# Performance work log

Hardware: AMD Instinct MI355X
Metric: run time of the kernel (lower is better)

The kernel has to match this reference:

```python
import jax, jax.numpy as jnp
import numpy as np

COST_LABELS = 2.0
COST_BBOX = 5.0
COST_GIOU = 2.0
NUM_HEADS = 7
NUM_CLASSES = 16


def setup_inputs() -> dict:
    key = jax.random.key(0)
    k0, k1, k2, k3 = jax.random.split(key, 4)
    bs, nq, nt = 16, 900, 100
    return {
        "pred_logits": jax.random.normal(k0, (NUM_HEADS, bs, nq, NUM_CLASSES), jnp.float32),
        "pred_boxes": jax.random.uniform(k1, (bs, nq, 4), jnp.float32),
        "tgt_boxes": jax.random.uniform(k2, (bs, nt, 4), jnp.float32),
        "tgt_labels": jax.random.randint(k3, (NUM_HEADS, bs, nt), 0, NUM_CLASSES),
    }


def box_cxcywh_to_xyxy(b):
    cx, cy, w, h = jnp.split(b, 4, axis=-1)
    return jnp.concatenate([cx - 0.5 * w, cy - 0.5 * h, cx + 0.5 * w, cy + 0.5 * h], axis=-1)


def generalized_box_iou(a, b):
    # a: [N,4] xyxy, b: [M,4] xyxy -> [N,M]
    area_a = (a[:, 2] - a[:, 0]) * (a[:, 3] - a[:, 1])
    area_b = (b[:, 2] - b[:, 0]) * (b[:, 3] - b[:, 1])
    lt = jnp.maximum(a[:, None, :2], b[None, :, :2])
    rb = jnp.minimum(a[:, None, 2:], b[None, :, 2:])
    wh = jnp.clip(rb - lt, 0.0)
    inter = wh[..., 0] * wh[..., 1]
    union = area_a[:, None] + area_b[None, :] - inter
    iou = inter / union
    lt_e = jnp.minimum(a[:, None, :2], b[None, :, :2])
    rb_e = jnp.maximum(a[:, None, 2:], b[None, :, 2:])
    wh_e = jnp.clip(rb_e - lt_e, 0.0)
    area = wh_e[..., 0] * wh_e[..., 1]
    return iou - (area - union) / area


@jax.jit
def compute_cost(pred_logits, pred_boxes, tgt_boxes, tgt_labels):
    bs, nq, _ = pred_boxes.shape
    out_bbox = pred_boxes.reshape(-1, 4)   # [N,4] cxcywh
    tgt_bbox = tgt_boxes.reshape(-1, 4)    # [M,4] cxcywh
    # L1 cdist
    cost_bbox = jnp.sum(jnp.abs(out_bbox[:, None, :] - tgt_bbox[None, :, :]), axis=-1)
    cost_giou = -generalized_box_iou(box_cxcywh_to_xyxy(out_bbox), box_cxcywh_to_xyxy(tgt_bbox))
    # label cost: sum over the 7 heads of -sigmoid(logits)[:, tgt_ids]
    probs = jax.nn.sigmoid(pred_logits.reshape(NUM_HEADS, -1, NUM_CLASSES))  # [7,N,C]
    ids = tgt_labels.reshape(NUM_HEADS, -1)                                   # [7,M]
    cost_labels = jnp.zeros_like(cost_bbox)
    for h in range(NUM_HEADS):  # small fixed loop, avoids a [7,N,M] intermediate
        cost_labels = cost_labels - probs[h][:, ids[h]]
    C = COST_BBOX * cost_bbox + COST_LABELS * cost_labels + COST_GIOU * cost_giou
    return C.reshape(bs, nq, -1)  # [bs, nq, bs*nt]


def _lsa(cost):
    """Jonker-Volgenant shortest augmenting path. cost: [r,c] with r<=c.
    Returns row2col: optimal column for each row (minimizes total cost)."""
    cost = np.asarray(cost, dtype=np.float64)
    r, c = cost.shape
    u = np.zeros(r + 1)
    v = np.zeros(c + 1)
    p = np.zeros(c + 1, np.int64)    # p[j] = row matched to column j (1-indexed)
    way = np.zeros(c + 1, np.int64)
    for i in range(1, r + 1):
        p[0] = i
        j0 = 0
        minv = np.full(c + 1, np.inf)
        used = np.zeros(c + 1, bool)
        while True:
            used[j0] = True
            i0 = p[j0]
            free = np.nonzero(~used)[0]  # unused columns (1..c)
            cur = cost[i0 - 1, free - 1] - u[i0] - v[free]
            better = cur < minv[free]
            minv[free] = np.where(better, cur, minv[free])
            way[free[better]] = j0
            k = np.argmin(minv[free])
            j1 = free[k]
            delta = minv[free][k]
            u[p[used]] += delta
            v[used] -= delta
            minv[free] -= delta
            j0 = j1
            if p[j0] == 0:
                break
        while j0:
            j1 = way[j0]
            p[j0] = p[j1]
            j0 = j1
    row2col = np.full(r, -1, np.int64)
    for j in range(1, c + 1):
        if p[j] > 0:
            row2col[p[j] - 1] = j - 1
    return row2col


def reference(pred_logits, pred_boxes, tgt_boxes, tgt_labels):
    C = compute_cost(pred_logits, pred_boxes, tgt_boxes, tgt_labels)  # [bs, nq, bs*nt]
    bs, nq, M = C.shape
    nt = M // bs
    Cn = np.asarray(C)
    out = np.zeros((bs, 2, nt), np.int64)
    for b in range(bs):
        sub = Cn[b, :, b * nt:(b + 1) * nt]  # [nq, nt] per-image block (mimics C.split(sizes))
        t2p = _lsa(sub.T)                    # for each target, its matched prediction
        order = np.argsort(t2p, kind="stable")  # scipy returns row indices sorted
        out[b, 0] = t2p[order]  # index_i: selected predictions (sorted)
        out[b, 1] = order       # index_j: corresponding targets
    return jnp.asarray(out)
```

## Files before the change

### kernel.cpp

```cpp
#include <hip/hip_runtime.h>
#include <hip/hip_bf16.h>
#include <math.h>

#define NQ 900
#define NT 100
#define BS 16
#define NH 7
#define NC 16
#define SLOTS 15

__global__ __launch_bounds__(256) void sig_transpose_kernel(const float* __restrict__ logits,
                                                            float* __restrict__ probsT) {
    const int hb = blockIdx.x;
    const float* src = logits + (size_t)hb * NQ * NC;
    float* dst = probsT + (size_t)hb * NC * NQ;
    __shared__ float tile[NC][NQ + 1];
    for (int e = threadIdx.x; e < NQ * NC; e += 256) {
        int q = e >> 4, c = e & 15;
        float x = src[e];
        tile[c][q] = 1.0f / (1.0f + expf(-x));
    }
    __syncthreads();
    for (int c = 0; c < NC; ++c)
        for (int q = threadIdx.x; q < NQ; q += 256)
            dst[c * NQ + q] = tile[c][q];
}

__global__ __launch_bounds__(256) void cost_kernel2(const float4* __restrict__ pboxes4,
                                                    const float4* __restrict__ tboxes4,
                                                    const int*    __restrict__ tlabels,
                                                    const float*  __restrict__ probsT,
                                                    float* __restrict__ costT) {
    int id = blockIdx.x * 256 + threadIdx.x;
    if (id >= BS * NT * NQ) return;
    int q = id % NQ;
    int t = (id / NQ) % NT;
    int b = id / (NQ * NT);

    float4 pb = pboxes4[b * NQ + q];
    float4 tb = tboxes4[b * NT + t];
    float px = pb.x, py = pb.y, pw = pb.z, ph = pb.w;
    float tx = tb.x, ty = tb.y, tw = tb.z, th = tb.w;

    float cost_bbox = fabsf(px - tx) + fabsf(py - ty) + fabsf(pw - tw) + fabsf(ph - th);

    float ax0 = px - 0.5f * pw, ay0 = py - 0.5f * ph;
    float ax1 = px + 0.5f * pw, ay1 = py + 0.5f * ph;
    float bx0 = tx - 0.5f * tw, by0 = ty - 0.5f * th;
    float bx1 = tx + 0.5f * tw, by1 = ty + 0.5f * th;
    float areaA = (ax1 - ax0) * (ay1 - ay0);
    float areaB = (bx1 - bx0) * (by1 - by0);
    float ltx = fmaxf(ax0, bx0), lty = fmaxf(ay0, by0);
    float rbx = fminf(ax1, bx1), rby = fminf(ay1, by1);
    float iw = fmaxf(rbx - ltx, 0.f), ih = fmaxf(rby - lty, 0.f);
    float inter = iw * ih;
    float uni = areaA + areaB - inter;
    float iou = inter / uni;
    float ex0 = fminf(ax0, bx0), ey0 = fminf(ay0, by0);
    float ex1 = fmaxf(ax1, bx1), ey1 = fmaxf(ay1, by1);
    float ew = fmaxf(ex1 - ex0, 0.f), eh = fmaxf(ey1 - ey0, 0.f);
    float earea = ew * eh;
    float giou = iou - (earea - uni) / earea;

    float ssum = 0.f;
    #pragma unroll
    for (int h = 0; h < NH; ++h) {
        int lab = tlabels[(h * BS + b) * NT + t];
        ssum += probsT[(size_t)((h * BS + b) * NC + lab) * NQ + q];
    }

    costT[(b * NT + t) * NQ + q] = 5.0f * cost_bbox - 2.0f * ssum - 2.0f * giou;
}

__global__ void cost_kernel_fb(const float* __restrict__ logits,
                               const float* __restrict__ pboxes,
                               const float* __restrict__ tboxes,
                               const int*   __restrict__ tlabels,
                               float* __restrict__ costT) {
    int id = blockIdx.x * blockDim.x + threadIdx.x;
    if (id >= BS * NT * NQ) return;
    int q = id % NQ;
    int t = (id / NQ) % NT;
    int b = id / (NQ * NT);

    const float* pb = pboxes + (b * NQ + q) * 4;
    const float* tb = tboxes + (b * NT + t) * 4;
    float px = pb[0], py = pb[1], pw = pb[2], ph = pb[3];
    float tx = tb[0], ty = tb[1], tw = tb[2], th = tb[3];

    float cost_bbox = fabsf(px - tx) + fabsf(py - ty) + fabsf(pw - tw) + fabsf(ph - th);

    float ax0 = px - 0.5f * pw, ay0 = py - 0.5f * ph;
    float ax1 = px + 0.5f * pw, ay1 = py + 0.5f * ph;
    float bx0 = tx - 0.5f * tw, by0 = ty - 0.5f * th;
    float bx1 = tx + 0.5f * tw, by1 = ty + 0.5f * th;
    float areaA = (ax1 - ax0) * (ay1 - ay0);
    float areaB = (bx1 - bx0) * (by1 - by0);
    float ltx = fmaxf(ax0, bx0), lty = fmaxf(ay0, by0);
    float rbx = fminf(ax1, bx1), rby = fminf(ay1, by1);
    float iw = fmaxf(rbx - ltx, 0.f), ih = fmaxf(rby - lty, 0.f);
    float inter = iw * ih;
    float uni = areaA + areaB - inter;
    float iou = inter / uni;
    float ex0 = fminf(ax0, bx0), ey0 = fminf(ay0, by0);
    float ex1 = fmaxf(ax1, bx1), ey1 = fmaxf(ay1, by1);
    float ew = fmaxf(ex1 - ex0, 0.f), eh = fmaxf(ey1 - ey0, 0.f);
    float earea = ew * eh;
    float giou = iou - (earea - uni) / earea;

    float ssum = 0.f;
    #pragma unroll
    for (int h = 0; h < NH; ++h) {
        int lab = tlabels[(h * BS + b) * NT + t];
        float x = logits[((h * BS + b) * NQ + q) * NC + lab];
        ssum += 1.0f / (1.0f + expf(-x));
    }

    costT[(b * NT + t) * NQ + q] = 5.0f * cost_bbox - 2.0f * ssum - 2.0f * giou;
}

__global__ __launch_bounds__(64) void lsa_kernel(const float* __restrict__ costT,
                                                 int* __restrict__ out) {
    const int b = blockIdx.x;
    const int lane = threadIdx.x;
    const float* cost = costT + b * NT * NQ;

    __shared__ double u_s[NT + 1];
    __shared__ int p_s[NQ + 1];
    __shared__ int way_s[NQ + 1];
    __shared__ int r2c[NT];
    __shared__ int jmin_s[NT];
    __shared__ int unass[NT];
    __shared__ int nun_s;

    for (int j = lane; j <= NQ; j += 64) p_s[j] = 0;
    __syncthreads();

    for (int base = 0; base < NT; base += 64) {
        int r = base + lane;
        if (r < NT) {
            const float4* row4 = (const float4*)(cost + (size_t)r * NQ);
            float m0 = INFINITY, m1 = INFINITY, m2 = INFINITY, m3 = INFINITY;
            int i0 = 0, i1 = 0, i2 = 0, i3 = 0;
            #pragma unroll 5
            for (int q4 = 0; q4 < NQ / 4; ++q4) {
                float4 cv = row4[q4];
                if (cv.x < m0) { m0 = cv.x; i0 = 4 * q4; }
                if (cv.y < m1) { m1 = cv.y; i1 = 4 * q4 + 1; }
                if (cv.z < m2) { m2 = cv.z; i2 = 4 * q4 + 2; }
                if (cv.w < m3) { m3 = cv.w; i3 = 4 * q4 + 3; }
            }
            float mv = m0; int mj = i0;
            if (m1 < mv || (m1 == mv && i1 < mj)) { mv = m1; mj = i1; }
            if (m2 < mv || (m2 == mv && i2 < mj)) { mv = m2; mj = i2; }
            if (m3 < mv || (m3 == mv && i3 < mj)) { mv = m3; mj = i3; }
            u_s[r + 1] = (double)mv;
            jmin_s[r] = mj;
        }
    }
    __syncthreads();

    if (lane == 0) {
        int nun = 0;
        for (int i = 1; i <= NT; ++i) {
            int j = jmin_s[i - 1] + 1;
            if (p_s[j] == 0) p_s[j] = i;
            else unass[nun++] = i;
        }
        nun_s = nun;
    }
    __syncthreads();
    const int nun = nun_s;

    double v[SLOTS], minv[SLOTS], ureg[SLOTS];
    int pof[SLOTS];
    #pragma unroll
    for (int k = 0; k < SLOTS; ++k) { v[k] = 0.0; ureg[k] = 0.0; pof[k] = 0; }
    const unsigned invalid = (lane < 4) ? 0u : (1u << 14);
    double u_c0 = 0.0;

    for (int ii = 0; ii < nun; ++ii) {
        const int i = unass[ii];
        #pragma unroll
        for (int k = 0; k < SLOTS; ++k) minv[k] = INFINITY;
        unsigned used = invalid;
        int j0 = 0;
        int i0 = i;

        while (true) {
            double u_i0 = u_s[i0];
            if (j0 != 0) {
                if (lane == ((j0 - 1) & 63)) {
                    int slot = (j0 - 1) >> 6;
                    used |= (1u << slot);
                    #pragma unroll
                    for (int k = 0; k < SLOTS; ++k)
                        if (slot == k) { pof[k] = i0; ureg[k] = u_i0; }
                }
            } else {
                if (lane == 0) u_c0 = u_i0;
            }

            const float* crow = cost + (size_t)(i0 - 1) * NQ;
            float c[SLOTS];
            #pragma unroll
            for (int k = 0; k < SLOTS - 1; ++k) c[k] = crow[lane + 64 * k];
            c[SLOTS - 1] = (lane < 4) ? crow[lane + 64 * (SLOTS - 1)] : 0.0f;

            double bv = INFINITY;
            int bj = 2048;
            #pragma unroll
            for (int k = 0; k < SLOTS; ++k) {
                if (!((used >> k) & 1u)) {
                    int j = 1 + lane + 64 * k;
                    double cur = ((double)c[k] - u_i0) - v[k];
                    if (cur < minv[k]) { minv[k] = cur; way_s[j] = j0; }
                    if (minv[k] < bv) { bv = minv[k]; bj = j; }
                }
            }
            #pragma unroll
            for (int off = 1; off < 64; off <<= 1) {
                double ov = __shfl_xor(bv, off);
                int oj = __shfl_xor(bj, off);
                if (ov < bv || (ov == bv && oj < bj)) { bv = ov; bj = oj; }
            }
            const double delta = bv;

            #pragma unroll
            for (int k = 0; k < SLOTS; ++k) {
                if ((used >> k) & 1u) { ureg[k] += delta; v[k] -= delta; }
                else                  { minv[k] -= delta; }
            }
            if (lane == 0) u_c0 += delta;

            j0 = bj;
            int pj = p_s[j0];
            if (pj == 0) break;
            i0 = pj;
        }

        __syncthreads();
        if (lane == 0) {
            int j = j0;
            while (j) {
                int jw = way_s[j];
                p_s[j] = (jw == 0) ? i : p_s[jw];
                j = jw;
            }
            u_s[i] = u_c0;
        }
        #pragma unroll
        for (int k = 0; k < SLOTS; ++k) {
            if (((used >> k) & 1u) && !((invalid >> k) & 1u)) u_s[pof[k]] = ureg[k];
        }
        __syncthreads();
    }

    for (int j = 1 + lane; j <= NQ; j += 64) {
        int pi = p_s[j];
        if (pi > 0) r2c[pi - 1] = j - 1;
    }
    __syncthreads();
    for (int t = lane; t < NT; t += 64) {
        int ccol = r2c[t];
        int rank = 0;
        for (int tt = 0; tt < NT; ++tt) rank += (r2c[tt] < ccol) ? 1 : 0;
        out[b * 2 * NT + rank] = ccol;
        out[b * 2 * NT + NT + rank] = t;
    }
}

extern "C" void kernel_launch(void* const* d_in, const int* in_sizes, int n_in,
                              void* d_out, int out_size, void* d_ws, size_t ws_size,
                              hipStream_t stream) {
    const float* logits  = (const float*)d_in[0];
    const float* pboxes  = (const float*)d_in[1];
    const float* tboxes  = (const float*)d_in[2];
    const int*   tlabels = (const int*)d_in[3];
    int* out = (int*)d_out;
    float* costT = (float*)d_ws;

    const size_t costT_elems  = (size_t)BS * NT * NQ;
    const size_t probsT_elems = (size_t)NH * BS * NC * NQ;
    const size_t need = (costT_elems + probsT_elems) * sizeof(float);

    const int total = BS * NT * NQ;
    if (ws_size >= need) {
        float* probsT = costT + costT_elems;
        sig_transpose_kernel<<<NH * BS, 256, 0, stream>>>(logits, probsT);
        cost_kernel2<<<(total + 255) / 256, 256, 0, stream>>>(
            (const float4*)pboxes, (const float4*)tboxes, tlabels, probsT, costT);
    } else {
        cost_kernel_fb<<<(total + 255) / 256, 256, 0, stream>>>(logits, pboxes, tboxes, tlabels, costT);
    }
    lsa_kernel<<<BS, 64, 0, stream>>>(costT, out);
}
```

Baseline: 128.5 us.

## Add auction-style augmenting row reduction before shortest-path LSA and fuse cost kernels

```diff
diff --git a/kernel.cpp b/kernel.cpp
--- a/kernel.cpp
+++ b/kernel.cpp
@@ -8,115 +8,57 @@
 #define NH 7
 #define NC 16
 #define SLOTS 15
-
-__global__ __launch_bounds__(256) void sig_transpose_kernel(const float* __restrict__ logits,
-                                                            float* __restrict__ probsT) {
-    const int hb = blockIdx.x;
-    const float* src = logits + (size_t)hb * NQ * NC;
-    float* dst = probsT + (size_t)hb * NC * NQ;
-    __shared__ float tile[NC][NQ + 1];
-    for (int e = threadIdx.x; e < NQ * NC; e += 256) {
-        int q = e >> 4, c = e & 15;
-        float x = src[e];
-        tile[c][q] = 1.0f / (1.0f + expf(-x));
-    }
-    __syncthreads();
-    for (int c = 0; c < NC; ++c)
-        for (int q = threadIdx.x; q < NQ; q += 256)
-            dst[c * NQ + q] = tile[c][q];
-}
-
-__global__ __launch_bounds__(256) void cost_kernel2(const float4* __restrict__ pboxes4,
-                                                    const float4* __restrict__ tboxes4,
-                                                    const int*    __restrict__ tlabels,
-                                                    const float*  __restrict__ probsT,
-                                                    float* __restrict__ costT) {
-    int id = blockIdx.x * 256 + threadIdx.x;
-    if (id >= BS * NT * NQ) return;
-    int q = id % NQ;
-    int t = (id / NQ) % NT;
-    int b = id / (NQ * NT);
-
-    float4 pb = pboxes4[b * NQ + q];
+#define MAXARR 512
+#define MAXTREE 8192
+
+__global__ __launch_bounds__(256) void cost_kernel(const float*  __restrict__ logits,
+                                                   const float4* __restrict__ pboxes4,
+                                                   const float4* __restrict__ tboxes4,
+                                                   const int*    __restrict__ tlabels,
+                                                   float* __restrict__ costT) {
+    const int bt = blockIdx.x;
+    const int b = bt / NT, t = bt % NT;
+
+    int lab[NH];
+    #pragma unroll
+    for (int h = 0; h < NH; ++h) lab[h] = tlabels[(h * BS + b) * NT + t];
+
     float4 tb = tboxes4[b * NT + t];
-    float px = pb.x, py = pb.y, pw = pb.z, ph = pb.w;
     float tx = tb.x, ty = tb.y, tw = tb.z, th = tb.w;
-
-    float cost_bbox = fabsf(px - tx) + fabsf(py - ty) + fabsf(pw - tw) + fabsf(ph - th);
-
-    float ax0 = px - 0.5f * pw, ay0 = py - 0.5f * ph;
-    float ax1 = px + 0.5f * pw, ay1 = py + 0.5f * ph;
     float bx0 = tx - 0.5f * tw, by0 = ty - 0.5f * th;
     float bx1 = tx + 0.5f * tw, by1 = ty + 0.5f * th;
-    float areaA = (ax1 - ax0) * (ay1 - ay0);
     float areaB = (bx1 - bx0) * (by1 - by0);
-    float ltx = fmaxf(ax0, bx0), lty = fmaxf(ay0, by0);
-    float rbx = fminf(ax1, bx1), rby = fminf(ay1, by1);
-    float iw = fmaxf(rbx - ltx, 0.f), ih = fmaxf(rby - lty, 0.f);
-    float inter = iw * ih;
-    float uni = areaA + areaB - inter;
-    float iou = inter / uni;
-    float ex0 = fminf(ax0, bx0), ey0 = fminf(ay0, by0);
-    float ex1 = fmaxf(ax1, bx1), ey1 = fmaxf(ay1, by1);
-    float ew = fmaxf(ex1 - ex0, 0.f), eh = fmaxf(ey1 - ey0, 0.f);
-    float earea = ew * eh;
-    float giou = iou - (earea - uni) / earea;
-
-    float ssum = 0.f;
-    #pragma unroll
-    for (int h = 0; h < NH; ++h) {
-        int lab = tlabels[(h * BS + b) * NT + t];
-        ssum += probsT[(size_t)((h * BS + b) * NC + lab) * NQ + q];
-    }
-
-    costT[(b * NT + t) * NQ + q] = 5.0f * cost_bbox - 2.0f * ssum - 2.0f * giou;
-}
-
-__global__ void cost_kernel_fb(const float* __restrict__ logits,
-                               const float* __restrict__ pboxes,
-                               const float* __restrict__ tboxes,
-                               const int*   __restrict__ tlabels,
-                               float* __restrict__ costT) {
-    int id = blockIdx.x * blockDim.x + threadIdx.x;
-    if (id >= BS * NT * NQ) return;
-    int q = id % NQ;
-    int t = (id / NQ) % NT;
-    int b = id / (NQ * NT);
-
-    const float* pb = pboxes + (b * NQ + q) * 4;
-    const float* tb = tboxes + (b * NT + t) * 4;
-    float px = pb[0], py = pb[1], pw = pb[2], ph = pb[3];
-    float tx = tb[0], ty = tb[1], tw = tb[2], th = tb[3];
-
-    float cost_bbox = fabsf(px - tx) + fabsf(py - ty) + fabsf(pw - tw) + fabsf(ph - th);
-
-    float ax0 = px - 0.5f * pw, ay0 = py - 0.5f * ph;
-    float ax1 = px + 0.5f * pw, ay1 = py + 0.5f * ph;
-    float bx0 = tx - 0.5f * tw, by0 = ty - 0.5f * th;
-    float bx1 = tx + 0.5f * tw, by1 = ty + 0.5f * th;
-    float areaA = (ax1 - ax0) * (ay1 - ay0);
-    float areaB = (bx1 - bx0) * (by1 - by0);
-    float ltx = fmaxf(ax0, bx0), lty = fmaxf(ay0, by0);
-    float rbx = fminf(ax1, bx1), rby = fminf(ay1, by1);
-    float iw = fmaxf(rbx - ltx, 0.f), ih = fmaxf(rby - lty, 0.f);
-    float inter = iw * ih;
-    float uni = areaA + areaB - inter;
-    float iou = inter / uni;
-    float ex0 = fminf(ax0, bx0), ey0 = fminf(ay0, by0);
-    float ex1 = fmaxf(ax1, bx1), ey1 = fmaxf(ay1, by1);
-    float ew = fmaxf(ex1 - ex0, 0.f), eh = fmaxf(ey1 - ey0, 0.f);
-    float earea = ew * eh;
-    float giou = iou - (earea - uni) / earea;
-
-    float ssum = 0.f;
-    #pragma unroll
-    for (int h = 0; h < NH; ++h) {
-        int lab = tlabels[(h * BS + b) * NT + t];
-        float x = logits[((h * BS + b) * NQ + q) * NC + lab];
-        ssum += 1.0f / (1.0f + expf(-x));
-    }
-
-    costT[(b * NT + t) * NQ + q] = 5.0f * cost_bbox - 2.0f * ssum - 2.0f * giou;
+
+    for (int q = threadIdx.x; q < NQ; q += 256) {
+        float4 pb = pboxes4[b * NQ + q];
+        float px = pb.x, py = pb.y, pw = pb.z, ph = pb.w;
+
+        float cost_bbox = fabsf(px - tx) + fabsf(py - ty) + fabsf(pw - tw) + fabsf(ph - th);
+
+        float ax0 = px - 0.5f * pw, ay0 = py - 0.5f * ph;
+        float ax1 = px + 0.5f * pw, ay1 = py + 0.5f * ph;
+        float areaA = (ax1 - ax0) * (ay1 - ay0);
+        float ltx = fmaxf(ax0, bx0), lty = fmaxf(ay0, by0);
+        float rbx = fminf(ax1, bx1), rby = fminf(ay1, by1);
+        float iw = fmaxf(rbx - ltx, 0.f), ih = fmaxf(rby - lty, 0.f);
+        float inter = iw * ih;
+        float uni = areaA + areaB - inter;
+        float iou = inter / uni;
+        float ex0 = fminf(ax0, bx0), ey0 = fminf(ay0, by0);
+        float ex1 = fmaxf(ax1, bx1), ey1 = fmaxf(ay1, by1);
+        float ew = fmaxf(ex1 - ex0, 0.f), eh = fmaxf(ey1 - ey0, 0.f);
+        float earea = ew * eh;
+        float giou = iou - (earea - uni) / earea;
+
+        float ssum = 0.f;
+        #pragma unroll
+        for (int h = 0; h < NH; ++h) {
+            float x = logits[(size_t)((h * BS + b) * NQ + q) * NC + lab[h]];
+            ssum += 1.0f / (1.0f + expf(-x));
+        }
+
+        costT[(b * NT + t) * NQ + q] = 5.0f * cost_bbox - 2.0f * ssum - 2.0f * giou;
+    }
 }
 
 __global__ __launch_bounds__(64) void lsa_kernel(const float* __restrict__ costT,
@@ -125,35 +67,36 @@
     const int lane = threadIdx.x;
     const float* cost = costT + b * NT * NQ;
 
+    __shared__ double2 pu[NQ + 1];
     __shared__ double u_s[NT + 1];
-    __shared__ int p_s[NQ + 1];
     __shared__ int way_s[NQ + 1];
-    __shared__ int r2c[NT];
+    __shared__ int x_s[NT + 1];
     __shared__ int jmin_s[NT];
     __shared__ int unass[NT];
+    __shared__ int r2c[NT];
     __shared__ int nun_s;
 
-    for (int j = lane; j <= NQ; j += 64) p_s[j] = 0;
+    for (int j = lane; j <= NQ; j += 64) pu[j] = make_double2(0.0, 0.0);
     __syncthreads();
 
     for (int base = 0; base < NT; base += 64) {
         int r = base + lane;
         if (r < NT) {
             const float4* row4 = (const float4*)(cost + (size_t)r * NQ);
-            float m0 = INFINITY, m1 = INFINITY, m2 = INFINITY, m3 = INFINITY;
+            float m0 = INFINITY, m1f = INFINITY, m2f = INFINITY, m3f = INFINITY;
             int i0 = 0, i1 = 0, i2 = 0, i3 = 0;
             #pragma unroll 5
             for (int q4 = 0; q4 < NQ / 4; ++q4) {
                 float4 cv = row4[q4];
-                if (cv.x < m0) { m0 = cv.x; i0 = 4 * q4; }
-                if (cv.y < m1) { m1 = cv.y; i1 = 4 * q4 + 1; }
-                if (cv.z < m2) { m2 = cv.z; i2 = 4 * q4 + 2; }
-                if (cv.w < m3) { m3 = cv.w; i3 = 4 * q4 + 3; }
+                if (cv.x < m0)  { m0 = cv.x;  i0 = 4 * q4; }
+                if (cv.y < m1f) { m1f = cv.y; i1 = 4 * q4 + 1; }
+                if (cv.z < m2f) { m2f = cv.z; i2 = 4 * q4 + 2; }
+                if (cv.w < m3f) { m3f = cv.w; i3 = 4 * q4 + 3; }
             }
             float mv = m0; int mj = i0;
-            if (m1 < mv || (m1 == mv && i1 < mj)) { mv = m1; mj = i1; }
-            if (m2 < mv || (m2 == mv && i2 < mj)) { mv = m2; mj = i2; }
-            if (m3 < mv || (m3 == mv && i3 < mj)) { mv = m3; mj = i3; }
+            if (m1f < mv || (m1f == mv && i1 < mj)) { mv = m1f; mj = i1; }
+            if (m2f < mv || (m2f == mv && i2 < mj)) { mv = m2f; mj = i2; }
+            if (m3f < mv || (m3f == mv && i3 < mj)) { mv = m3f; mj = i3; }
             u_s[r + 1] = (double)mv;
             jmin_s[r] = mj;
         }
@@ -164,8 +107,8 @@
         int nun = 0;
         for (int i = 1; i <= NT; ++i) {
             int j = jmin_s[i - 1] + 1;
-            if (p_s[j] == 0) p_s[j] = i;
-            else unass[nun++] = i;
+            if ((int)pu[j].y == 0) { pu[j] = make_double2(u_s[i], (double)i); x_s[i] = j; }
+            else                   { x_s[i] = 0; unass[nun++] = i; }
         }
         nun_s = nun;
     }
@@ -179,16 +122,80 @@
     const unsigned invalid = (lane < 4) ? 0u : (1u << 14);
     double u_c0 = 0.0;
 
-    for (int ii = 0; ii < nun; ++ii) {
+    {
+        int steps = 0;
+        for (int idx = 0; idx < nun; ++idx) {
+            int i = unass[idx];
+            while (i != 0 && steps < MAXARR) {
+                ++steps;
+                const float* crow = cost + (size_t)(i - 1) * NQ;
+                float c[SLOTS];
+                #pragma unroll
+                for (int k = 0; k < SLOTS - 1; ++k) c[k] = crow[lane + 64 * k];
+                c[SLOTS - 1] = (lane < 4) ? crow[lane + 64 * (SLOTS - 1)] : 0.0f;
+
+                double m1 = INFINITY, m2 = INFINITY;
+                int j1 = 2048;
+                #pragma unroll
+                for (int k = 0; k < SLOTS; ++k) {
+                    if (!((invalid >> k) & 1u)) {
+                        int j = 1 + lane + 64 * k;
+                        double d = (double)c[k] - v[k];
+                        if (d < m1 || (d == m1 && j < j1)) { m2 = m1; m1 = d; j1 = j; }
+                        else if (d < m2) m2 = d;
+                    }
+                }
+                #pragma unroll
+                for (int off = 1; off < 64; off <<= 1) {
+                    double om1 = __shfl_xor(m1, off);
+                    double om2 = __shfl_xor(m2, off);
+                    int oj1 = __shfl_xor(j1, off);
+                    if (om1 < m1 || (om1 == m1 && oj1 < j1)) { m2 = fmin(m1, om2); m1 = om1; j1 = oj1; }
+                    else { m2 = fmin(m2, om1); }
+                }
+
+                double2 t = pu[j1];
+                int k1 = (int)t.y;
+                if (m1 == m2 && k1 != 0) break;
+
+                if (m1 < m2) {
+                    if (lane == ((j1 - 1) & 63)) {
+                        int slot = (j1 - 1) >> 6;
+                        #pragma unroll
+                        for (int k = 0; k < SLOTS; ++k) if (k == slot) v[k] -= (m2 - m1);
+                    }
+                }
+                if (lane == 0) {
+                    u_s[i] = m2;
+                    pu[j1] = make_double2(m2, (double)i);
+                    x_s[i] = j1;
+                    if (k1) x_s[k1] = 0;
+                }
+                i = k1;
+            }
+        }
+    }
+    __syncthreads();
+
+    if (lane == 0) {
+        int n2 = 0;
+        for (int i = 1; i <= NT; ++i) if (x_s[i] == 0) unass[n2++] = i;
+        nun_s = n2;
+    }
+    __syncthreads();
+    const int nun2 = nun_s;
+
+    for (int ii = 0; ii < nun2; ++ii) {
         const int i = unass[ii];
         #pragma unroll
         for (int k = 0; k < SLOTS; ++k) minv[k] = INFINITY;
         unsigned used = invalid;
         int j0 = 0;
         int i0 = i;
-
-        while (true) {
-            double u_i0 = u_s[i0];
+        double u_i0 = u_s[i];
+        int guard = 0;
+
+        while (guard++ < MAXTREE) {
             if (j0 != 0) {
                 if (lane == ((j0 - 1) & 63)) {
                     int slot = (j0 - 1) >> 6;
@@ -233,31 +240,38 @@
             }
             if (lane == 0) u_c0 += delta;
 
+            double2 t = pu[bj];
             j0 = bj;
-            int pj = p_s[j0];
-            if (pj == 0) break;
-            i0 = pj;
-        }
-
+            i0 = (int)t.y;
+            u_i0 = t.x;
+            if (i0 == 0) break;
+        }
+
+        __syncthreads();
+        #pragma unroll
+        for (int k = 0; k < SLOTS; ++k) {
+            if (((used >> k) & 1u) && !((invalid >> k) & 1u)) {
+                int j = 1 + lane + 64 * k;
+                u_s[pof[k]] = ureg[k];
+                pu[j] = make_double2(ureg[k], (double)pof[k]);
+            }
+        }
         __syncthreads();
         if (lane == 0) {
+            u_s[i] = u_c0;
             int j = j0;
             while (j) {
                 int jw = way_s[j];
-                p_s[j] = (jw == 0) ? i : p_s[jw];
+                double2 t2 = (jw == 0) ? make_double2(u_c0, (double)i) : pu[jw];
+                pu[j] = t2;
                 j = jw;
             }
-            u_s[i] = u_c0;
-        }
-        #pragma unroll
-        for (int k = 0; k < SLOTS; ++k) {
-            if (((used >> k) & 1u) && !((invalid >> k) & 1u)) u_s[pof[k]] = ureg[k];
         }
         __syncthreads();
     }
 
     for (int j = 1 + lane; j <= NQ; j += 64) {
-        int pi = p_s[j];
+        int pi = (int)pu[j].y;
         if (pi > 0) r2c[pi - 1] = j - 1;
     }
     __syncthreads();
@@ -280,18 +294,7 @@
     int* out = (int*)d_out;
     float* costT = (float*)d_ws;
 
-    const size_t costT_elems  = (size_t)BS * NT * NQ;
-    const size_t probsT_elems = (size_t)NH * BS * NC * NQ;
-    const size_t need = (costT_elems + probsT_elems) * sizeof(float);
-
-    const int total = BS * NT * NQ;
-    if (ws_size >= need) {
-        float* probsT = costT + costT_elems;
-        sig_transpose_kernel<<<NH * BS, 256, 0, stream>>>(logits, probsT);
-        cost_kernel2<<<(total + 255) / 256, 256, 0, stream>>>(
-            (const float4*)pboxes, (const float4*)tboxes, tlabels, probsT, costT);
-    } else {
-        cost_kernel_fb<<<(total + 255) / 256, 256, 0, stream>>>(logits, pboxes, tboxes, tlabels, costT);
-    }
+    cost_kernel<<<BS * NT, 256, 0, stream>>>(logits, (const float4*)pboxes,
+                                             (const float4*)tboxes, tlabels, costT);
     lsa_kernel<<<BS, 64, 0, stream>>>(costT, out);
 }
```

After: 147.3 us. +14.6%, slower.

## Add auction-style reduction-transfer pre-pass and per-target cost kernel blocks

Applied to the files above, without the earlier changes.

```diff
diff --git a/kernel.cpp b/kernel.cpp
--- a/kernel.cpp
+++ b/kernel.cpp
@@ -8,6 +8,8 @@
 #define NH 7
 #define NC 16
 #define SLOTS 15
+#define MAXROUNDS 32
+#define MAXTREE 8192
 
 __global__ __launch_bounds__(256) void sig_transpose_kernel(const float* __restrict__ logits,
                                                             float* __restrict__ probsT) {
@@ -26,21 +28,71 @@
             dst[c * NQ + q] = tile[c][q];
 }
 
-__global__ __launch_bounds__(256) void cost_kernel2(const float4* __restrict__ pboxes4,
-                                                    const float4* __restrict__ tboxes4,
-                                                    const int*    __restrict__ tlabels,
-                                                    const float*  __restrict__ probsT,
-                                                    float* __restrict__ costT) {
-    int id = blockIdx.x * 256 + threadIdx.x;
+__global__ __launch_bounds__(256) void cost_kernel_bt(const float4* __restrict__ pboxes4,
+                                                      const float4* __restrict__ tboxes4,
+                                                      const int*    __restrict__ tlabels,
+                                                      const float*  __restrict__ probsT,
+                                                      float* __restrict__ costT) {
+    const int bt = blockIdx.x;
+    const int b = bt / NT, t = bt % NT;
+
+    const float* prow[NH];
+    #pragma unroll
+    for (int h = 0; h < NH; ++h) {
+        int lab = tlabels[(h * BS + b) * NT + t];
+        prow[h] = probsT + (size_t)((h * BS + b) * NC + lab) * NQ;
+    }
+
+    float4 tb = tboxes4[b * NT + t];
+    float tx = tb.x, ty = tb.y, tw = tb.z, th = tb.w;
+    float bx0 = tx - 0.5f * tw, by0 = ty - 0.5f * th;
+    float bx1 = tx + 0.5f * tw, by1 = ty + 0.5f * th;
+    float areaB = (bx1 - bx0) * (by1 - by0);
+
+    for (int q = threadIdx.x; q < NQ; q += 256) {
+        float4 pb = pboxes4[b * NQ + q];
+        float px = pb.x, py = pb.y, pw = pb.z, ph = pb.w;
+
+        float cost_bbox = fabsf(px - tx) + fabsf(py - ty) + fabsf(pw - tw) + fabsf(ph - th);
+
+        float ax0 = px - 0.5f * pw, ay0 = py - 0.5f * ph;
+        float ax1 = px + 0.5f * pw, ay1 = py + 0.5f * ph;
+        float areaA = (ax1 - ax0) * (ay1 - ay0);
+        float ltx = fmaxf(ax0, bx0), lty = fmaxf(ay0, by0);
+        float rbx = fminf(ax1, bx1), rby = fminf(ay1, by1);
+        float iw = fmaxf(rbx - ltx, 0.f), ih = fmaxf(rby - lty, 0.f);
+        float inter = iw * ih;
+        float uni = areaA + areaB - inter;
+        float iou = inter / uni;
+        float ex0 = fminf(ax0, bx0), ey0 = fminf(ay0, by0);
+        float ex1 = fmaxf(ax1, bx1), ey1 = fmaxf(ay1, by1);
+        float ew = fmaxf(ex1 - ex0, 0.f), eh = fmaxf(ey1 - ey0, 0.f);
+        float earea = ew * eh;
+        float giou = iou - (earea - uni) / earea;
+
+        float ssum = 0.f;
+        #pragma unroll
+        for (int h = 0; h < NH; ++h) ssum += prow[h][q];
+
+        costT[(b * NT + t) * NQ + q] = 5.0f * cost_bbox - 2.0f * ssum - 2.0f * giou;
+    }
+}
+
+__global__ void cost_kernel_fb(const float* __restrict__ logits,
+                               const float* __restrict__ pboxes,
+                               const float* __restrict__ tboxes,
+                               const int*   __restrict__ tlabels,
+                               float* __restrict__ costT) {
+    int id = blockIdx.x * blockDim.x + threadIdx.x;
     if (id >= BS * NT * NQ) return;
     int q = id % NQ;
     int t = (id / NQ) % NT;
     int b = id / (NQ * NT);
 
-    float4 pb = pboxes4[b * NQ + q];
-    float4 tb = tboxes4[b * NT + t];
-    float px = pb.x, py = pb.y, pw = pb.z, ph = pb.w;
-    float tx = tb.x, ty = tb.y, tw = tb.z, th = tb.w;
+    const float* pb = pboxes + (b * NQ + q) * 4;
+    const float* tb = tboxes + (b * NT + t) * 4;
+    float px = pb[0], py = pb[1], pw = pb[2], ph = pb[3];
+    float tx = tb[0], ty = tb[1], tw = tb[2], th = tb[3];
 
     float cost_bbox = fabsf(px - tx) + fabsf(py - ty) + fabsf(pw - tw) + fabsf(ph - th);
 
@@ -66,52 +118,6 @@
     #pragma unroll
     for (int h = 0; h < NH; ++h) {
         int lab = tlabels[(h * BS + b) * NT + t];
-        ssum += probsT[(size_t)((h * BS + b) * NC + lab) * NQ + q];
-    }
-
-    costT[(b * NT + t) * NQ + q] = 5.0f * cost_bbox - 2.0f * ssum - 2.0f * giou;
-}
-
-__global__ void cost_kernel_fb(const float* __restrict__ logits,
-                               const float* __restrict__ pboxes,
-                               const float* __restrict__ tboxes,
-                               const int*   __restrict__ tlabels,
-                               float* __restrict__ costT) {
-    int id = blockIdx.x * blockDim.x + threadIdx.x;
-    if (id >= BS * NT * NQ) return;
-    int q = id % NQ;
-    int t = (id / NQ) % NT;
-    int b = id / (NQ * NT);
-
-    const float* pb = pboxes + (b * NQ + q) * 4;
-    const float* tb = tboxes + (b * NT + t) * 4;
-    float px = pb[0], py = pb[1], pw = pb[2], ph = pb[3];
-    float tx = tb[0], ty = tb[1], tw = tb[2], th = tb[3];
-
-    float cost_bbox = fabsf(px - tx) + fabsf(py - ty) + fabsf(pw - tw) + fabsf(ph - th);
-
-    float ax0 = px - 0.5f * pw, ay0 = py - 0.5f * ph;
-    float ax1 = px + 0.5f * pw, ay1 = py + 0.5f * ph;
-    float bx0 = tx - 0.5f * tw, by0 = ty - 0.5f * th;
-    float bx1 = tx + 0.5f * tw, by1 = ty + 0.5f * th;
-    float areaA = (ax1 - ax0) * (ay1 - ay0);
-    float areaB = (bx1 - bx0) * (by1 - by0);
-    float ltx = fmaxf(ax0, bx0), lty = fmaxf(ay0, by0);
-    float rbx = fminf(ax1, bx1), rby = fminf(ay1, by1);
-    float iw = fmaxf(rbx - ltx, 0.f), ih = fmaxf(rby - lty, 0.f);
-    float inter = iw * ih;
-    float uni = areaA + areaB - inter;
-    float iou = inter / uni;
-    float ex0 = fminf(ax0, bx0), ey0 = fminf(ay0, by0);
-    float ex1 = fmaxf(ax1, bx1), ey1 = fmaxf(ay1, by1);
-    float ew = fmaxf(ex1 - ex0, 0.f), eh = fmaxf(ey1 - ey0, 0.f);
-    float earea = ew * eh;
-    float giou = iou - (earea - uni) / earea;
-
-    float ssum = 0.f;
-    #pragma unroll
-    for (int h = 0; h < NH; ++h) {
-        int lab = tlabels[(h * BS + b) * NT + t];
         float x = logits[((h * BS + b) * NQ + q) * NC + lab];
         ssum += 1.0f / (1.0f + expf(-x));
     }
@@ -125,52 +131,68 @@
     const int lane = threadIdx.x;
     const float* cost = costT + b * NT * NQ;
 
+    __shared__ double2 pu[NQ + 1];
     __shared__ double u_s[NT + 1];
-    __shared__ int p_s[NQ + 1];
     __shared__ int way_s[NQ + 1];
+    __shared__ int x_s[NT + 1];
+    __shared__ int p_w[NQ + 1];
+    __shared__ int touched[NQ + 1];
+    __shared__ int jmin_s[NT];
+    __shared__ int listA[NT], listB[NT];
+    __shared__ double2 scan_mm[NT];
+    __shared__ int scan_j1[NT];
     __shared__ int r2c[NT];
-    __shared__ int jmin_s[NT];
-    __shared__ int unass[NT];
-    __shared__ int nun_s;
-
-    for (int j = lane; j <= NQ; j += 64) p_s[j] = 0;
+    __shared__ int cnt_s;
+
+    for (int j = lane; j <= NQ; j += 64) {
+        pu[j] = make_double2(0.0, 0.0);
+        p_w[j] = 0x7fffffff;
+        touched[j] = -1;
+    }
+    if (lane == 0) cnt_s = 0;
     __syncthreads();
 
     for (int base = 0; base < NT; base += 64) {
         int r = base + lane;
         if (r < NT) {
             const float4* row4 = (const float4*)(cost + (size_t)r * NQ);
-            float m0 = INFINITY, m1 = INFINITY, m2 = INFINITY, m3 = INFINITY;
+            float m0 = INFINITY, m1f = INFINITY, m2f = INFINITY, m3f = INFINITY;
             int i0 = 0, i1 = 0, i2 = 0, i3 = 0;
             #pragma unroll 5
             for (int q4 = 0; q4 < NQ / 4; ++q4) {
                 float4 cv = row4[q4];
-                if (cv.x < m0) { m0 = cv.x; i0 = 4 * q4; }
-                if (cv.y < m1) { m1 = cv.y; i1 = 4 * q4 + 1; }
-                if (cv.z < m2) { m2 = cv.z; i2 = 4 * q4 + 2; }
-                if (cv.w < m3) { m3 = cv.w; i3 = 4 * q4 + 3; }
+                if (cv.x < m0)  { m0 = cv.x;  i0 = 4 * q4; }
+                if (cv.y < m1f) { m1f = cv.y; i1 = 4 * q4 + 1; }
+                if (cv.z < m2f) { m2f = cv.z; i2 = 4 * q4 + 2; }
+                if (cv.w < m3f) { m3f = cv.w; i3 = 4 * q4 + 3; }
             }
             float mv = m0; int mj = i0;
-            if (m1 < mv || (m1 == mv && i1 < mj)) { mv = m1; mj = i1; }
-            if (m2 < mv || (m2 == mv && i2 < mj)) { mv = m2; mj = i2; }
-            if (m3 < mv || (m3 == mv && i3 < mj)) { mv = m3; mj = i3; }
+            if (m1f < mv || (m1f == mv && i1 < mj)) { mv = m1f; mj = i1; }
+            if (m2f < mv || (m2f == mv && i2 < mj)) { mv = m2f; mj = i2; }
+            if (m3f < mv || (m3f == mv && i3 < mj)) { mv = m3f; mj = i3; }
             u_s[r + 1] = (double)mv;
             jmin_s[r] = mj;
-        }
-    }
-    __syncthreads();
-
-    if (lane == 0) {
-        int nun = 0;
-        for (int i = 1; i <= NT; ++i) {
-            int j = jmin_s[i - 1] + 1;
-            if (p_s[j] == 0) p_s[j] = i;
-            else unass[nun++] = i;
-        }
-        nun_s = nun;
-    }
-    __syncthreads();
-    const int nun = nun_s;
+            atomicMin(&p_w[mj + 1], r + 1);
+        }
+    }
+    __syncthreads();
+
+    for (int base = 0; base < NT; base += 64) {
+        int r = base + lane;
+        if (r < NT) {
+            int j = jmin_s[r] + 1;
+            if (p_w[j] == r + 1) {
+                x_s[r + 1] = j;
+                pu[j] = make_double2(u_s[r + 1], (double)(r + 1));
+            } else {
+                x_s[r + 1] = 0;
+                int pos = atomicAdd(&cnt_s, 1);
+                listA[pos] = r + 1;
+            }
+        }
+    }
+    __syncthreads();
+    int nfree = cnt_s;
 
     double v[SLOTS], minv[SLOTS], ureg[SLOTS];
     int pof[SLOTS];
@@ -179,16 +201,112 @@
     const unsigned invalid = (lane < 4) ? 0u : (1u << 14);
     double u_c0 = 0.0;
 
-    for (int ii = 0; ii < nun; ++ii) {
-        const int i = unass[ii];
+    int* curL = listA;
+    int* nxtL = listB;
+    for (int round = 0; round < MAXROUNDS && nfree > 0; ++round) {
+        for (int idx = 0; idx < nfree; idx += 2) {
+            const int iA = curL[idx];
+            const bool hasB = (idx + 1) < nfree;
+            const int iB = hasB ? curL[idx + 1] : iA;
+            const float* rowA = cost + (size_t)(iA - 1) * NQ;
+            const float* rowB = cost + (size_t)(iB - 1) * NQ;
+            float cA[SLOTS], cB[SLOTS];
+            #pragma unroll
+            for (int k = 0; k < SLOTS - 1; ++k) cA[k] = rowA[lane + 64 * k];
+            cA[SLOTS - 1] = (lane < 4) ? rowA[lane + 64 * (SLOTS - 1)] : 0.0f;
+            #pragma unroll
+            for (int k = 0; k < SLOTS - 1; ++k) cB[k] = rowB[lane + 64 * k];
+            cB[SLOTS - 1] = (lane < 4) ? rowB[lane + 64 * (SLOTS - 1)] : 0.0f;
+
+            {
+                double m1 = INFINITY, m2 = INFINITY; int j1 = 2048;
+                #pragma unroll
+                for (int k = 0; k < SLOTS; ++k) {
+                    if (!((invalid >> k) & 1u)) {
+                        int j = 1 + lane + 64 * k;
+                        double d = (double)cA[k] - v[k];
+                        if (d < m1 || (d == m1 && j < j1)) { m2 = m1; m1 = d; j1 = j; }
+                        else if (d < m2) m2 = d;
+                    }
+                }
+                #pragma unroll
+                for (int off = 1; off < 64; off <<= 1) {
+                    double om1 = __shfl_xor(m1, off);
+                    double om2 = __shfl_xor(m2, off);
+                    int oj1 = __shfl_xor(j1, off);
+                    if (om1 < m1 || (om1 == m1 && oj1 < j1)) { m2 = fmin(m1, om2); m1 = om1; j1 = oj1; }
+                    else m2 = fmin(m2, om1);
+                }
+                if (lane == 0) { scan_mm[idx] = make_double2(m1, m2); scan_j1[idx] = j1; }
+            }
+            if (hasB) {
+                double m1 = INFINITY, m2 = INFINITY; int j1 = 2048;
+                #pragma unroll
+                for (int k = 0; k < SLOTS; ++k) {
+                    if (!((invalid >> k) & 1u)) {
+                        int j = 1 + lane + 64 * k;
+                        double d = (double)cB[k] - v[k];
+                        if (d < m1 || (d == m1 && j < j1)) { m2 = m1; m1 = d; j1 = j; }
+                        else if (d < m2) m2 = d;
+                    }
+                }
+                #pragma unroll
+                for (int off = 1; off < 64; off <<= 1) {
+                    double om1 = __shfl_xor(m1, off);
+                    double om2 = __shfl_xor(m2, off);
+                    int oj1 = __shfl_xor(j1, off);
+                    if (om1 < m1 || (om1 == m1 && oj1 < j1)) { m2 = fmin(m1, om2); m1 = om1; j1 = oj1; }
+                    else m2 = fmin(m2, om1);
+                }
+                if (lane == 0) { scan_mm[idx + 1] = make_double2(m1, m2); scan_j1[idx + 1] = j1; }
+            }
+        }
+
+        int nfree2 = 0;
+        for (int idx = 0; idx < nfree; ++idx) {
+            int i = curL[idx];
+            double2 mm = scan_mm[idx];
+            int j1 = scan_j1[idx];
+            if (touched[j1] == round) {
+                if (lane == 0) nxtL[nfree2] = i;
+                ++nfree2;
+                continue;
+            }
+            int k1 = (int)pu[j1].y;
+            if (lane == 0) touched[j1] = round;
+            int sl = (j1 - 1) >> 6;
+            if (lane == ((j1 - 1) & 63)) {
+                double dv = mm.y - mm.x;
+                #pragma unroll
+                for (int k = 0; k < SLOTS; ++k) if (k == sl) v[k] -= dv;
+            }
+            if (lane == 0) {
+                u_s[i] = mm.y;
+                pu[j1] = make_double2(mm.y, (double)i);
+                x_s[i] = j1;
+                if (k1) x_s[k1] = 0;
+            }
+            if (k1) {
+                if (lane == 0) nxtL[nfree2] = k1;
+                ++nfree2;
+            }
+        }
+        int* tmp = curL; curL = nxtL; nxtL = tmp;
+        nfree = nfree2;
+    }
+    __syncthreads();
+
+    for (int ii = 0; ii < nfree; ++ii) {
+        const int i = curL[ii];
         #pragma unroll
         for (int k = 0; k < SLOTS; ++k) minv[k] = INFINITY;
         unsigned used = invalid;
         int j0 = 0;
         int i0 = i;
-
-        while (true) {
-            double u_i0 = u_s[i0];
+        double u_i0 = u_s[i];
+        int guard = 0;
+
+        while (guard++ < MAXTREE) {
             if (j0 != 0) {
                 if (lane == ((j0 - 1) & 63)) {
                     int slot = (j0 - 1) >> 6;
@@ -233,31 +351,38 @@
             }
             if (lane == 0) u_c0 += delta;
 
+            double2 t = pu[bj];
             j0 = bj;
-            int pj = p_s[j0];
-            if (pj == 0) break;
-            i0 = pj;
-        }
-
+            i0 = (int)t.y;
+            u_i0 = t.x;
+            if (i0 == 0) break;
+        }
+
+        __syncthreads();
+        #pragma unroll
+        for (int k = 0; k < SLOTS; ++k) {
+            if (((used >> k) & 1u) && !((invalid >> k) & 1u)) {
+                int j = 1 + lane + 64 * k;
+                u_s[pof[k]] = ureg[k];
+                pu[j] = make_double2(ureg[k], (double)pof[k]);
+            }
+        }
         __syncthreads();
         if (lane == 0) {
+            u_s[i] = u_c0;
             int j = j0;
             while (j) {
                 int jw = way_s[j];
-                p_s[j] = (jw == 0) ? i : p_s[jw];
+                double2 t2 = (jw == 0) ? make_double2(u_c0, (double)i) : pu[jw];
+                pu[j] = t2;
                 j = jw;
             }
-            u_s[i] = u_c0;
-        }
-        #pragma unroll
-        for (int k = 0; k < SLOTS; ++k) {
-            if (((used >> k) & 1u) && !((invalid >> k) & 1u)) u_s[pof[k]] = ureg[k];
         }
         __syncthreads();
     }
 
     for (int j = 1 + lane; j <= NQ; j += 64) {
-        int pi = p_s[j];
+        int pi = (int)pu[j].y;
         if (pi > 0) r2c[pi - 1] = j - 1;
     }
     __syncthreads();
@@ -284,13 +409,13 @@
     const size_t probsT_elems = (size_t)NH * BS * NC * NQ;
     const size_t need = (costT_elems + probsT_elems) * sizeof(float);
 
-    const int total = BS * NT * NQ;
     if (ws_size >= need) {
         float* probsT = costT + costT_elems;
         sig_transpose_kernel<<<NH * BS, 256, 0, stream>>>(logits, probsT);
-        cost_kernel2<<<(total + 255) / 256, 256, 0, stream>>>(
-            (const float4*)pboxes, (const float4*)tboxes, tlabels, probsT, costT);
+        cost_kernel_bt<<<BS * NT, 256, 0, stream>>>((const float4*)pboxes,
+                                                    (const float4*)tboxes, tlabels, probsT, costT);
     } else {
+        const int total = BS * NT * NQ;
         cost_kernel_fb<<<(total + 255) / 256, 256, 0, stream>>>(logits, pboxes, tboxes, tlabels, costT);
     }
     lsa_kernel<<<BS, 64, 0, stream>>>(costT, out);
```

New measurement: 133.8 us. 1.04x slower.

## Pack assignment and dual into shared double2; parallelize greedy init; per-target cost blocks

Applied to the files above, without the earlier changes.

```diff
diff --git a/kernel.cpp b/kernel.cpp
--- a/kernel.cpp
+++ b/kernel.cpp
@@ -8,6 +8,7 @@
 #define NH 7
 #define NC 16
 #define SLOTS 15
+#define MAXTREE 8192
 
 __global__ __launch_bounds__(256) void sig_transpose_kernel(const float* __restrict__ logits,
                                                             float* __restrict__ probsT) {
@@ -26,21 +27,71 @@
             dst[c * NQ + q] = tile[c][q];
 }
 
-__global__ __launch_bounds__(256) void cost_kernel2(const float4* __restrict__ pboxes4,
-                                                    const float4* __restrict__ tboxes4,
-                                                    const int*    __restrict__ tlabels,
-                                                    const float*  __restrict__ probsT,
-                                                    float* __restrict__ costT) {
-    int id = blockIdx.x * 256 + threadIdx.x;
+__global__ __launch_bounds__(256) void cost_kernel_bt(const float4* __restrict__ pboxes4,
+                                                      const float4* __restrict__ tboxes4,
+                                                      const int*    __restrict__ tlabels,
+                                                      const float*  __restrict__ probsT,
+                                                      float* __restrict__ costT) {
+    const int bt = blockIdx.x;
+    const int b = bt / NT, t = bt % NT;
+
+    const float* prow[NH];
+    #pragma unroll
+    for (int h = 0; h < NH; ++h) {
+        int lab = tlabels[(h * BS + b) * NT + t];
+        prow[h] = probsT + (size_t)((h * BS + b) * NC + lab) * NQ;
+    }
+
+    float4 tb = tboxes4[b * NT + t];
+    float tx = tb.x, ty = tb.y, tw = tb.z, th = tb.w;
+    float bx0 = tx - 0.5f * tw, by0 = ty - 0.5f * th;
+    float bx1 = tx + 0.5f * tw, by1 = ty + 0.5f * th;
+    float areaB = (bx1 - bx0) * (by1 - by0);
+
+    for (int q = threadIdx.x; q < NQ; q += 256) {
+        float4 pb = pboxes4[b * NQ + q];
+        float px = pb.x, py = pb.y, pw = pb.z, ph = pb.w;
+
+        float cost_bbox = fabsf(px - tx) + fabsf(py - ty) + fabsf(pw - tw) + fabsf(ph - th);
+
+        float ax0 = px - 0.5f * pw, ay0 = py - 0.5f * ph;
+        float ax1 = px + 0.5f * pw, ay1 = py + 0.5f * ph;
+        float areaA = (ax1 - ax0) * (ay1 - ay0);
+        float ltx = fmaxf(ax0, bx0), lty = fmaxf(ay0, by0);
+        float rbx = fminf(ax1, bx1), rby = fminf(ay1, by1);
+        float iw = fmaxf(rbx - ltx, 0.f), ih = fmaxf(rby - lty, 0.f);
+        float inter = iw * ih;
+        float uni = areaA + areaB - inter;
+        float iou = inter / uni;
+        float ex0 = fminf(ax0, bx0), ey0 = fminf(ay0, by0);
+        float ex1 = fmaxf(ax1, bx1), ey1 = fmaxf(ay1, by1);
+        float ew = fmaxf(ex1 - ex0, 0.f), eh = fmaxf(ey1 - ey0, 0.f);
+        float earea = ew * eh;
+        float giou = iou - (earea - uni) / earea;
+
+        float ssum = 0.f;
+        #pragma unroll
+        for (int h = 0; h < NH; ++h) ssum += prow[h][q];
+
+        costT[(b * NT + t) * NQ + q] = 5.0f * cost_bbox - 2.0f * ssum - 2.0f * giou;
+    }
+}
+
+__global__ void cost_kernel_fb(const float* __restrict__ logits,
+                               const float* __restrict__ pboxes,
+                               const float* __restrict__ tboxes,
+                               const int*   __restrict__ tlabels,
+                               float* __restrict__ costT) {
+    int id = blockIdx.x * blockDim.x + threadIdx.x;
     if (id >= BS * NT * NQ) return;
     int q = id % NQ;
     int t = (id / NQ) % NT;
     int b = id / (NQ * NT);
 
-    float4 pb = pboxes4[b * NQ + q];
-    float4 tb = tboxes4[b * NT + t];
-    float px = pb.x, py = pb.y, pw = pb.z, ph = pb.w;
-    float tx = tb.x, ty = tb.y, tw = tb.z, th = tb.w;
+    const float* pb = pboxes + (b * NQ + q) * 4;
+    const float* tb = tboxes + (b * NT + t) * 4;
+    float px = pb[0], py = pb[1], pw = pb[2], ph = pb[3];
+    float tx = tb[0], ty = tb[1], tw = tb[2], th = tb[3];
 
     float cost_bbox = fabsf(px - tx) + fabsf(py - ty) + fabsf(pw - tw) + fabsf(ph - th);
 
@@ -66,52 +117,6 @@
     #pragma unroll
     for (int h = 0; h < NH; ++h) {
         int lab = tlabels[(h * BS + b) * NT + t];
-        ssum += probsT[(size_t)((h * BS + b) * NC + lab) * NQ + q];
-    }
-
-    costT[(b * NT + t) * NQ + q] = 5.0f * cost_bbox - 2.0f * ssum - 2.0f * giou;
-}
-
-__global__ void cost_kernel_fb(const float* __restrict__ logits,
-                               const float* __restrict__ pboxes,
-                               const float* __restrict__ tboxes,
-                               const int*   __restrict__ tlabels,
-                               float* __restrict__ costT) {
-    int id = blockIdx.x * blockDim.x + threadIdx.x;
-    if (id >= BS * NT * NQ) return;
-    int q = id % NQ;
-    int t = (id / NQ) % NT;
-    int b = id / (NQ * NT);
-
-    const float* pb = pboxes + (b * NQ + q) * 4;
-    const float* tb = tboxes + (b * NT + t) * 4;
-    float px = pb[0], py = pb[1], pw = pb[2], ph = pb[3];
-    float tx = tb[0], ty = tb[1], tw = tb[2], th = tb[3];
-
-    float cost_bbox = fabsf(px - tx) + fabsf(py - ty) + fabsf(pw - tw) + fabsf(ph - th);
-
-    float ax0 = px - 0.5f * pw, ay0 = py - 0.5f * ph;
-    float ax1 = px + 0.5f * pw, ay1 = py + 0.5f * ph;
-    float bx0 = tx - 0.5f * tw, by0 = ty - 0.5f * th;
-    float bx1 = tx + 0.5f * tw, by1 = ty + 0.5f * th;
-    float areaA = (ax1 - ax0) * (ay1 - ay0);
-    float areaB = (bx1 - bx0) * (by1 - by0);
-    float ltx = fmaxf(ax0, bx0), lty = fmaxf(ay0, by0);
-    float rbx = fminf(ax1, bx1), rby = fminf(ay1, by1);
-    float iw = fmaxf(rbx - ltx, 0.f), ih = fmaxf(rby - lty, 0.f);
-    float inter = iw * ih;
-    float uni = areaA + areaB - inter;
-    float iou = inter / uni;
-    float ex0 = fminf(ax0, bx0), ey0 = fminf(ay0, by0);
-    float ex1 = fmaxf(ax1, bx1), ey1 = fmaxf(ay1, by1);
-    float ew = fmaxf(ex1 - ex0, 0.f), eh = fmaxf(ey1 - ey0, 0.f);
-    float earea = ew * eh;
-    float giou = iou - (earea - uni) / earea;
-
-    float ssum = 0.f;
-    #pragma unroll
-    for (int h = 0; h < NH; ++h) {
-        int lab = tlabels[(h * BS + b) * NT + t];
         float x = logits[((h * BS + b) * NQ + q) * NC + lab];
         ssum += 1.0f / (1.0f + expf(-x));
     }
@@ -125,52 +130,72 @@
     const int lane = threadIdx.x;
     const float* cost = costT + b * NT * NQ;
 
+    __shared__ double2 pu[NQ + 1];
     __shared__ double u_s[NT + 1];
-    __shared__ int p_s[NQ + 1];
     __shared__ int way_s[NQ + 1];
+    __shared__ int p_w[NQ + 1];
+    __shared__ int jmin_s[NT];
+    __shared__ int listA[NT];
     __shared__ int r2c[NT];
-    __shared__ int jmin_s[NT];
-    __shared__ int unass[NT];
-    __shared__ int nun_s;
-
-    for (int j = lane; j <= NQ; j += 64) p_s[j] = 0;
-    __syncthreads();
-
-    for (int base = 0; base < NT; base += 64) {
-        int r = base + lane;
+    __shared__ int cnt_s;
+
+    for (int j = lane; j <= NQ; j += 64) {
+        pu[j] = make_double2(0.0, 0.0);
+        p_w[j] = 0x7fffffff;
+    }
+    __syncthreads();
+
+    bool lostA = false, lostB = false;
+    #pragma unroll
+    for (int pass = 0; pass < 2; ++pass) {
+        int r = pass * 64 + lane;
         if (r < NT) {
             const float4* row4 = (const float4*)(cost + (size_t)r * NQ);
-            float m0 = INFINITY, m1 = INFINITY, m2 = INFINITY, m3 = INFINITY;
+            float m0 = INFINITY, m1f = INFINITY, m2f = INFINITY, m3f = INFINITY;
             int i0 = 0, i1 = 0, i2 = 0, i3 = 0;
             #pragma unroll 5
             for (int q4 = 0; q4 < NQ / 4; ++q4) {
                 float4 cv = row4[q4];
-                if (cv.x < m0) { m0 = cv.x; i0 = 4 * q4; }
-                if (cv.y < m1) { m1 = cv.y; i1 = 4 * q4 + 1; }
-                if (cv.z < m2) { m2 = cv.z; i2 = 4 * q4 + 2; }
-                if (cv.w < m3) { m3 = cv.w; i3 = 4 * q4 + 3; }
+                if (cv.x < m0)  { m0 = cv.x;  i0 = 4 * q4; }
+                if (cv.y < m1f) { m1f = cv.y; i1 = 4 * q4 + 1; }
+                if (cv.z < m2f) { m2f = cv.z; i2 = 4 * q4 + 2; }
+                if (cv.w < m3f) { m3f = cv.w; i3 = 4 * q4 + 3; }
             }
             float mv = m0; int mj = i0;
-            if (m1 < mv || (m1 == mv && i1 < mj)) { mv = m1; mj = i1; }
-            if (m2 < mv || (m2 == mv && i2 < mj)) { mv = m2; mj = i2; }
-            if (m3 < mv || (m3 == mv && i3 < mj)) { mv = m3; mj = i3; }
+            if (m1f < mv || (m1f == mv && i1 < mj)) { mv = m1f; mj = i1; }
+            if (m2f < mv || (m2f == mv && i2 < mj)) { mv = m2f; mj = i2; }
+            if (m3f < mv || (m3f == mv && i3 < mj)) { mv = m3f; mj = i3; }
             u_s[r + 1] = (double)mv;
             jmin_s[r] = mj;
+            atomicMin(&p_w[mj + 1], r + 1);
         }
     }
     __syncthreads();
 
+    {
+        int rA = lane;
+        int j = jmin_s[rA] + 1;
+        if (p_w[j] == rA + 1) pu[j] = make_double2(u_s[rA + 1], (double)(rA + 1));
+        else lostA = true;
+    }
+    if (lane < NT - 64) {
+        int rB = 64 + lane;
+        int j = jmin_s[rB] + 1;
+        if (p_w[j] == rB + 1) pu[j] = make_double2(u_s[rB + 1], (double)(rB + 1));
+        else lostB = true;
+    }
+    unsigned long long mA = __ballot(lostA);
+    unsigned long long mB = __ballot(lostB);
     if (lane == 0) {
-        int nun = 0;
-        for (int i = 1; i <= NT; ++i) {
-            int j = jmin_s[i - 1] + 1;
-            if (p_s[j] == 0) p_s[j] = i;
-            else unass[nun++] = i;
-        }
-        nun_s = nun;
-    }
-    __syncthreads();
-    const int nun = nun_s;
+        int n = 0;
+        unsigned long long m = mA;
+        while (m) { int l = __ffsll((long long)m) - 1; listA[n++] = l + 1; m &= m - 1; }
+        m = mB;
+        while (m) { int l = __ffsll((long long)m) - 1; listA[n++] = 64 + l + 1; m &= m - 1; }
+        cnt_s = n;
+    }
+    __syncthreads();
+    const int nfree = cnt_s;
 
     double v[SLOTS], minv[SLOTS], ureg[SLOTS];
     int pof[SLOTS];
@@ -179,16 +204,17 @@
     const unsigned invalid = (lane < 4) ? 0u : (1u << 14);
     double u_c0 = 0.0;
 
-    for (int ii = 0; ii < nun; ++ii) {
-        const int i = unass[ii];
+    for (int ii = 0; ii < nfree; ++ii) {
+        const int i = listA[ii];
         #pragma unroll
         for (int k = 0; k < SLOTS; ++k) minv[k] = INFINITY;
         unsigned used = invalid;
         int j0 = 0;
         int i0 = i;
-
-        while (true) {
-            double u_i0 = u_s[i0];
+        double u_i0 = u_s[i];
+        int guard = 0;
+
+        while (guard++ < MAXTREE) {
             if (j0 != 0) {
                 if (lane == ((j0 - 1) & 63)) {
                     int slot = (j0 - 1) >> 6;
@@ -226,38 +252,46 @@
             }
             const double delta = bv;
 
+            double2 t = pu[bj];
+
             #pragma unroll
             for (int k = 0; k < SLOTS; ++k) {
+                minv[k] -= delta;
                 if ((used >> k) & 1u) { ureg[k] += delta; v[k] -= delta; }
-                else                  { minv[k] -= delta; }
             }
             if (lane == 0) u_c0 += delta;
 
             j0 = bj;
-            int pj = p_s[j0];
-            if (pj == 0) break;
-            i0 = pj;
+            i0 = (int)t.y;
+            u_i0 = t.x;
+            if (i0 == 0) break;
         }
 
+        __syncthreads();
+        #pragma unroll
+        for (int k = 0; k < SLOTS; ++k) {
+            if (((used >> k) & 1u) && !((invalid >> k) & 1u)) {
+                int j = 1 + lane + 64 * k;
+                u_s[pof[k]] = ureg[k];
+                pu[j] = make_double2(ureg[k], (double)pof[k]);
+            }
+        }
         __syncthreads();
         if (lane == 0) {
+            u_s[i] = u_c0;
             int j = j0;
             while (j) {
                 int jw = way_s[j];
-                p_s[j] = (jw == 0) ? i : p_s[jw];
+                double2 t2 = (jw == 0) ? make_double2(u_c0, (double)i) : pu[jw];
+                pu[j] = t2;
                 j = jw;
             }
-            u_s[i] = u_c0;
-        }
-        #pragma unroll
-        for (int k = 0; k < SLOTS; ++k) {
-            if (((used >> k) & 1u) && !((invalid >> k) & 1u)) u_s[pof[k]] = ureg[k];
         }
         __syncthreads();
     }
 
     for (int j = 1 + lane; j <= NQ; j += 64) {
-        int pi = p_s[j];
+        int pi = (int)pu[j].y;
         if (pi > 0) r2c[pi - 1] = j - 1;
     }
     __syncthreads();
@@ -284,13 +318,13 @@
     const size_t probsT_elems = (size_t)NH * BS * NC * NQ;
     const size_t need = (costT_elems + probsT_elems) * sizeof(float);
 
-    const int total = BS * NT * NQ;
     if (ws_size >= need) {
         float* probsT = costT + costT_elems;
         sig_transpose_kernel<<<NH * BS, 256, 0, stream>>>(logits, probsT);
-        cost_kernel2<<<(total + 255) / 256, 256, 0, stream>>>(
-            (const float4*)pboxes, (const float4*)tboxes, tlabels, probsT, costT);
+        cost_kernel_bt<<<BS * NT, 256, 0, stream>>>((const float4*)pboxes,
+                                                    (const float4*)tboxes, tlabels, probsT, costT);
     } else {
+        const int total = BS * NT * NQ;
         cost_kernel_fb<<<(total + 255) / 256, 256, 0, stream>>>(logits, pboxes, tboxes, tlabels, costT);
     }
     lsa_kernel<<<BS, 64, 0, stream>>>(costT, out);
```

New measurement: 125.0 us. -2.7%, faster.
